# Kernel tuning notes

Hardware: AMD Instinct MI355X
Metric: run time of the kernel (lower is better)

## Reference

```python
import jax, jax.numpy as jnp
import numpy as np

# Module constants (from init_kwargs / MoELayer branch for n_experts=8)
D_MODEL = 512
D_FF = 2048
N_HEADS = 8
N_EXPERTS = 8
TOP_K = 2
CAPACITY_FACTOR = 1.6  # n_experts > 6 branch
BATCH = 4096
SEQ = 16  # 4x4 board
LN_EPS = 1e-5


def setup_inputs() -> dict:
    key = jax.random.key(0)
    ks = jax.random.split(key, 24)
    s = 0.02
    d, f, e = D_MODEL, D_FF, N_EXPERTS
    inp = {
        'x': jax.random.normal(ks[0], (BATCH, SEQ, d), dtype=jnp.float32),
        'ln1_g': jnp.ones((d,), jnp.float32), 'ln1_b': jnp.zeros((d,), jnp.float32),
        'ln2_g': jnp.ones((d,), jnp.float32), 'ln2_b': jnp.zeros((d,), jnp.float32),
        # Linear weights stored [in, out] (equivalent to torch W.T)
        'wq': jax.random.normal(ks[1], (d, d)) * s, 'bq': jnp.zeros((d,)),
        'wk': jax.random.normal(ks[2], (d, d)) * s, 'bk': jnp.zeros((d,)),
        'wv': jax.random.normal(ks[3], (d, d)) * s, 'bv': jnp.zeros((d,)),
        'wo': jax.random.normal(ks[4], (d, d)) * s, 'bo': jnp.zeros((d,)),
        'router_w': jax.random.normal(ks[5], (d, e)) * s, 'router_b': jnp.zeros((e,)),
        'w1': jax.random.normal(ks[6], (e, d, f)) * s, 'b1': jnp.zeros((e, f)),
        'w2': jax.random.normal(ks[7], (e, f, d)) * s, 'b2': jnp.zeros((e, d)),
    }
    return inp


def _layernorm(x, g, b):
    mu = x.mean(-1, keepdims=True)
    var = ((x - mu) ** 2).mean(-1, keepdims=True)
    return (x - mu) * jax.lax.rsqrt(var + LN_EPS) * g + b


def _moe(xf, router_w, router_b, w1, b1, w2, b2):
    # xf: [T, D]
    T = xf.shape[0]
    probs = jax.nn.softmax(xf @ router_w + router_b, axis=-1)  # [T, E]
    _, topk_idx = jax.lax.top_k(probs, TOP_K)                  # [T, K]
    capacity = int(np.ceil(T * CAPACITY_FACTOR / N_EXPERTS))
    out = jnp.zeros_like(xf)
    tok = jnp.arange(T)
    for i in range(N_EXPERTS):
        mask = (topk_idx == i).any(-1)                 # token routed to expert i
        pos = jnp.where(mask, tok, T)                  # sentinel T for unrouted
        sel = jnp.sort(pos)[:capacity]                 # first `capacity` routed tokens, in token order
        xi = xf[jnp.minimum(sel, T - 1)]               # gather (padded rows unused)
        hi = jax.nn.gelu(xi @ w1[i] + b1[i], approximate=False)
        yi = hi @ w2[i] + b2[i]
        # scatter; OOB sentinel indices are dropped. Later experts overwrite
        # earlier ones for tokens routed to multiple experts (matches torch).
        out = out.at[sel].set(yi, mode='drop')
    return out


def reference(x, ln1_g, ln1_b, ln2_g, ln2_b, wq, bq, wk, bk, wv, bv, wo, bo,
              router_w, router_b, w1, b1, w2, b2):
    B, S, D = x.shape
    dk = D // N_HEADS
    # --- attention sublayer ---
    h = _layernorm(x, ln1_g, ln1_b)
    q = (h @ wq + bq).reshape(B, S, N_HEADS, dk)
    k = (h @ wk + bk).reshape(B, S, N_HEADS, dk)
    v = (h @ wv + bv).reshape(B, S, N_HEADS, dk)
    scores = jnp.einsum('bqhd,bkhd->bhqk', q, k) / np.sqrt(dk).astype(np.float32)
    attn = jax.nn.softmax(scores, axis=-1)
    ctx = jnp.einsum('bhqk,bkhd->bqhd', attn, v).reshape(B, S, D)
    x = x + ctx @ wo + bo
    # --- MoE sublayer ---
    h2 = _layernorm(x, ln2_g, ln2_b)
    moe_out = _moe(h2.reshape(-1, D), router_w, router_b, w1, b1, w2, b2)
    return x + moe_out.reshape(B, S, D)
```

## Files before the change

kernel.cpp:

```cpp
#include <hip/hip_runtime.h>
#include <hip/hip_bf16.h>
#include <math.h>

typedef unsigned short u16;
typedef unsigned int u32;
typedef _Float16 f16;
typedef __attribute__((ext_vector_type(8))) _Float16 f16x8;
typedef __attribute__((ext_vector_type(8))) short short8;
typedef __attribute__((ext_vector_type(4))) float f32x4;

#define TTOK 65536
#define QTOK 16384
#define CAP 13108
#define CAPP 13184

#define MFMA16(a, b, c) __builtin_amdgcn_mfma_f32_16x16x32_f16(a, b, c, 0, 0, 0)
#define MFMAB(a, b, c) __builtin_amdgcn_mfma_f32_16x16x32_bf16(a, b, c, 0, 0, 0)
#define LO_SCALE 2.44140625e-4f

#define SWZF(r) (((r) & 3) ^ ((((r) >> 2) & 1) << 1))

__device__ __forceinline__ u16 f2bf(float f) {
  union { float f; u32 u; } v; v.f = f;
  u32 r = v.u + 0x7fffu + ((v.u >> 16) & 1u);
  return (u16)(r >> 16);
}
__device__ __forceinline__ u16 f16b(f16 h) {
  union { f16 h; u16 u; } v; v.h = h; return v.u;
}
__device__ __forceinline__ f16 b2h(u16 u) {
  union { u16 s; f16 h; } v; v.s = u; return v.h;
}
__device__ __forceinline__ float gelu_f(float x) {
  float z = fabsf(x) * 0.70710678118654752f;
  float t = __builtin_amdgcn_rcpf(1.0f + 0.3275911f * z);
  float p = t * (0.254829592f + t * (-0.284496736f + t * (1.421413741f
          + t * (-1.453152027f + t * 1.061405429f))));
  float er = 1.0f - p * __expf(-z * z);
  er = (x < 0.0f) ? -er : er;
  return 0.5f * x * (1.0f + er);
}
__device__ __forceinline__ void gl16(const u16* g, u16* l) {
  __builtin_amdgcn_global_load_lds(
      (const __attribute__((address_space(1))) u32*)(const void*)g,
      (__attribute__((address_space(3))) u32*)(void*)l, 16, 0, 0);
}

__global__ __launch_bounds__(256) void prep1_kernel(
    const float* __restrict__ wq, const float* __restrict__ wk,
    const float* __restrict__ wv, const float* __restrict__ wo,
    const float* __restrict__ rw,
    u16* __restrict__ whi, u16* __restrict__ wlo, float* __restrict__ rwt)
{
  const int z = blockIdx.z;
  int idx = blockIdx.x * 256 + threadIdx.x;
  if (z == 4) {
    if (idx < 4096) {
      int n = idx >> 9, k = idx & 511;
      rwt[idx] = rw[k * 8 + n];
    }
    return;
  }
  const float* src = (z == 0) ? wq : (z == 1) ? wk : (z == 2) ? wv : wo;
  int n = idx >> 9, k = idx & 511;
  float v = src[k * 512 + n];
  f16 h = (f16)v;
  f16 l = (f16)((v - (float)h) * 4096.0f);
  whi[z * 262144 + idx] = f16b(h);
  wlo[z * 262144 + idx] = f16b(l);
}

__global__ __launch_bounds__(256) void prep2_kernel(
    const float* __restrict__ w1, const float* __restrict__ w2,
    u16* __restrict__ w1t, u16* __restrict__ w2t)
{
  __shared__ float tS[64][65];
  const int z = blockIdx.z;
  const float* src; u16* dst; int R, C;
  if (z < 8) { src = w1 + (size_t)z * 1048576; dst = w1t + (size_t)z * 1048576; R = 512; C = 2048; }
  else       { src = w2 + (size_t)(z - 8) * 1048576; dst = w2t + (size_t)(z - 8) * 1048576; R = 2048; C = 512; }
  const int tc = C >> 6;
  const int r0 = (blockIdx.x / tc) * 64, c0 = (blockIdx.x % tc) * 64;
  const int tid = threadIdx.x;
  #pragma unroll
  for (int j = 0; j < 16; ++j) {
    int idx = j * 256 + tid;
    int r = idx >> 6, c = idx & 63;
    tS[r][c] = src[(size_t)(r0 + r) * C + c0 + c];
  }
  __syncthreads();
  #pragma unroll
  for (int j = 0; j < 16; ++j) {
    int idx = j * 256 + tid;
    int c = idx >> 6, r = idx & 63;
    dst[(size_t)(c0 + c) * R + r0 + r] = f2bf(tS[r][c]);
  }
}

__global__ __launch_bounds__(256) void ln1_kernel(
    const float* __restrict__ x, const float* __restrict__ g,
    const float* __restrict__ b, u16* __restrict__ hh, u16* __restrict__ hl)
{
  const int row = blockIdx.x * 4 + (threadIdx.x >> 6);
  const int lane = threadIdx.x & 63;
  const float* xr = x + (size_t)row * 512 + lane * 8;
  float4 a = *(const float4*)xr;
  float4 c = *(const float4*)(xr + 4);
  double s1 = (double)a.x + a.y + a.z + a.w + c.x + c.y + c.z + c.w;
  double s2 = (double)a.x * a.x + (double)a.y * a.y + (double)a.z * a.z + (double)a.w * a.w
            + (double)c.x * c.x + (double)c.y * c.y + (double)c.z * c.z + (double)c.w * c.w;
  #pragma unroll
  for (int off = 32; off; off >>= 1) {
    s1 += __shfl_xor(s1, off, 64);
    s2 += __shfl_xor(s2, off, 64);
  }
  double mu = s1 * (1.0 / 512.0);
  double var = s2 * (1.0 / 512.0) - mu * mu;
  double rs = 1.0 / sqrt(var + 1e-5);
  float4 ga = *(const float4*)(g + lane * 8);
  float4 gb = *(const float4*)(g + lane * 8 + 4);
  float4 ba = *(const float4*)(b + lane * 8);
  float4 bb = *(const float4*)(b + lane * 8 + 4);
  float vv[8] = {a.x, a.y, a.z, a.w, c.x, c.y, c.z, c.w};
  float gg[8] = {ga.x, ga.y, ga.z, ga.w, gb.x, gb.y, gb.z, gb.w};
  float cc[8] = {ba.x, ba.y, ba.z, ba.w, bb.x, bb.y, bb.z, bb.w};
  u16 oh[8], ol[8];
  #pragma unroll
  for (int j = 0; j < 8; ++j) {
    float t = (float)(((double)vv[j] - mu) * rs);
    float n0 = t * gg[j] + cc[j];
    f16 h = (f16)n0;
    oh[j] = f16b(h);
    ol[j] = f16b((f16)((n0 - (float)h) * 4096.0f));
  }
  size_t base = (size_t)row * 512 + lane * 8;
  *(short8*)(hh + base) = *(const short8*)oh;
  *(short8*)(hl + base) = *(const short8*)ol;
}

__device__ __forceinline__ void qkv_body(
    int lid, u16* SMb,
    const u16* __restrict__ hh, const u16* __restrict__ hl,
    const u16* __restrict__ whi, const u16* __restrict__ wlo,
    const float* __restrict__ bq, const float* __restrict__ bk,
    const float* __restrict__ bv, u32* __restrict__ qkvh, int M0)
{
  const int tid = threadIdx.x;
  const int lane = tid & 63, w = tid >> 6;
  const int c8 = lid & 7, kk = lid >> 3;
  const int rt = c8 * 16 + kk / 12;
  const int ct = kk % 12;
  const int col0 = ct * 128;
  const int row0 = rt * 128;
  const int wr = w >> 2, wc = w & 3;
  const int lr = lane & 15, lkq = lane >> 4;
  const int sx = (lkq ^ SWZF(lr)) * 8;
  const int lrow = lane >> 2;
  const int lcs = ((lane & 3) ^ SWZF(lrow)) * 8;

  const u16* gsrc[4];
  int loff[4];
  #pragma unroll
  for (int j = 0; j < 4; ++j) {
    const int q = w * 4 + j;
    loff[j] = q * 512;
    if (q < 8)       gsrc[j] = hh + (size_t)(M0 + row0 + q * 16 + lrow) * 512 + lcs;
    else if (q < 16) gsrc[j] = hl + (size_t)(M0 + row0 + (q - 8) * 16 + lrow) * 512 + lcs;
    else if (q < 24) gsrc[j] = whi + (size_t)(col0 + (q - 16) * 16 + lrow) * 512 + lcs;
    else             gsrc[j] = wlo + (size_t)(col0 + (q - 24) * 16 + lrow) * 512 + lcs;
  }

  f32x4 acch[4][2], accl[4][2];
  #pragma unroll
  for (int m = 0; m < 4; ++m)
    #pragma unroll
    for (int n = 0; n < 2; ++n) {
      f32x4 zz = {0.f, 0.f, 0.f, 0.f};
      acch[m][n] = zz; accl[m][n] = zz;
    }

  #pragma unroll
  for (int j = 0; j < 4; ++j) gl16(gsrc[j], &SMb[loff[j]]);
  #pragma unroll
  for (int j = 0; j < 4; ++j) gl16(gsrc[j] + 32, &SMb[16384 + loff[j]]);

  for (int kc = 0; kc < 16; ++kc) {
    if (kc == 15) asm volatile("s_waitcnt vmcnt(0)" ::: "memory");
    else          asm volatile("s_waitcnt vmcnt(4)" ::: "memory");
    __builtin_amdgcn_s_barrier();
    __builtin_amdgcn_sched_barrier(0);
    const u16* S = &SMb[(kc & 1) * 16384];
    f16x8 ah[4], al[4], bh[2], bl[2];
    #pragma unroll
    for (int m = 0; m < 4; ++m) {
      int r = wr * 64 + m * 16 + lr;
      ah[m] = *(const f16x8*)&S[r * 32 + sx];
      al[m] = *(const f16x8*)&S[4096 + r * 32 + sx];
    }
    #pragma unroll
    for (int n = 0; n < 2; ++n) {
      int c = wc * 32 + n * 16 + lr;
      bh[n] = *(const f16x8*)&S[8192 + c * 32 + sx];
      bl[n] = *(const f16x8*)&S[12288 + c * 32 + sx];
    }
    #pragma unroll
    for (int m = 0; m < 4; ++m)
      #pragma unroll
      for (int n = 0; n < 2; ++n) {
        acch[m][n] = MFMA16(ah[m], bh[n], acch[m][n]);
        accl[m][n] = MFMA16(ah[m], bl[n], accl[m][n]);
        accl[m][n] = MFMA16(al[m], bh[n], accl[m][n]);
      }
    __builtin_amdgcn_s_barrier();
    __builtin_amdgcn_sched_barrier(0);
    if (kc + 2 < 16) {
      #pragma unroll
      for (int j = 0; j < 4; ++j) gl16(gsrc[j] + (kc + 2) * 32, &SMb[(kc & 1) * 16384 + loff[j]]);
    }
  }
  #pragma unroll
  for (int m = 0; m < 4; ++m)
    #pragma unroll
    for (int n = 0; n < 2; ++n) {
      int col = col0 + wc * 32 + n * 16 + lr;
      float bb = (col < 512) ? bq[col] : (col < 1024) ? bk[col - 512] : bv[col - 1024];
      #pragma unroll
      for (int r = 0; r < 4; ++r) {
        int row = row0 + wr * 64 + m * 16 + lkq * 4 + r;
        float val = acch[m][n][r] + accl[m][n][r] * LO_SCALE + bb;
        f16 vh = (f16)val;
        f16 vl = (f16)((val - (float)vh) * 4096.0f);
        qkvh[(size_t)row * 1536 + col] = (u32)f16b(vh) | ((u32)f16b(vl) << 16);
      }
    }
}

__global__ __launch_bounds__(512, 2) void qkv_gemm_kernel(
    const u16* __restrict__ hh, const u16* __restrict__ hl,
    const u16* __restrict__ whi, const u16* __restrict__ wlo,
    const float* __restrict__ bq, const float* __restrict__ bk,
    const float* __restrict__ bv, u32* __restrict__ qkvh, int M0)
{
  __shared__ alignas(16) u16 SM[2][16384];
  qkv_body(blockIdx.x + 12 * blockIdx.y, &SM[0][0],
           hh, hl, whi, wlo, bq, bk, bv, qkvh, M0);
}

__device__ __forceinline__ void wo_body(
    int lid, u16* SMb,
    const u16* __restrict__ cth, const u16* __restrict__ ctl,
    const u16* __restrict__ whi, const u16* __restrict__ wlo,
    const float* __restrict__ bo, const float* __restrict__ x,
    float* __restrict__ dout, int M0)
{
  const int tid = threadIdx.x;
  const int lane = tid & 63, w = tid >> 6;
  const int c8 = lid & 7, kk = lid >> 3;
  const int rt = c8 * 16 + (kk >> 2), ct = kk & 3;
  const int col0 = ct * 128;
  const int row0 = rt * 128;
  const int wr = w >> 2, wc = w & 3;
  const int lr = lane & 15, lkq = lane >> 4;
  const int sx = (lkq ^ SWZF(lr)) * 8;
  const int lrow = lane >> 2;
  const int lcs = ((lane & 3) ^ SWZF(lrow)) * 8;

  const u16* wh3 = whi + 3 * 262144;
  const u16* wl3 = wlo + 3 * 262144;

  const u16* gsrc[4];
  int loff[4];
  #pragma unroll
  for (int j = 0; j < 4; ++j) {
    const int q = w * 4 + j;
    loff[j] = q * 512;
    if (q < 8)       gsrc[j] = cth + (size_t)(row0 + q * 16 + lrow) * 512 + lcs;
    else if (q < 16) gsrc[j] = ctl + (size_t)(row0 + (q - 8) * 16 + lrow) * 512 + lcs;
    else if (q < 24) gsrc[j] = wh3 + (size_t)(col0 + (q - 16) * 16 + lrow) * 512 + lcs;
    else             gsrc[j] = wl3 + (size_t)(col0 + (q - 24) * 16 + lrow) * 512 + lcs;
  }

  f32x4 acch[4][2], accl[4][2];
  #pragma unroll
  for (int m = 0; m < 4; ++m)
    #pragma unroll
    for (int n = 0; n < 2; ++n) {
      f32x4 zz = {0.f, 0.f, 0.f, 0.f};
      acch[m][n] = zz; accl[m][n] = zz;
    }

  #pragma unroll
  for (int j = 0; j < 4; ++j) gl16(gsrc[j], &SMb[loff[j]]);
  #pragma unroll
  for (int j = 0; j < 4; ++j) gl16(gsrc[j] + 32, &SMb[16384 + loff[j]]);

  for (int kc = 0; kc < 16; ++kc) {
    if (kc == 15) asm volatile("s_waitcnt vmcnt(0)" ::: "memory");
    else          asm volatile("s_waitcnt vmcnt(4)" ::: "memory");
    __builtin_amdgcn_s_barrier();
    __builtin_amdgcn_sched_barrier(0);
    const u16* S = &SMb[(kc & 1) * 16384];
    f16x8 ah[4], al[4], bh[2], bl[2];
    #pragma unroll
    for (int m = 0; m < 4; ++m) {
      int r = wr * 64 + m * 16 + lr;
      ah[m] = *(const f16x8*)&S[r * 32 + sx];
      al[m] = *(const f16x8*)&S[4096 + r * 32 + sx];
    }
    #pragma unroll
    for (int n = 0; n < 2; ++n) {
      int c = wc * 32 + n * 16 + lr;
      bh[n] = *(const f16x8*)&S[8192 + c * 32 + sx];
      bl[n] = *(const f16x8*)&S[12288 + c * 32 + sx];
    }
    #pragma unroll
    for (int m = 0; m < 4; ++m)
      #pragma unroll
      for (int n = 0; n < 2; ++n) {
        acch[m][n] = MFMA16(ah[m], bh[n], acch[m][n]);
        accl[m][n] = MFMA16(ah[m], bl[n], accl[m][n]);
        accl[m][n] = MFMA16(al[m], bh[n], accl[m][n]);
      }
    __builtin_amdgcn_s_barrier();
    __builtin_amdgcn_sched_barrier(0);
    if (kc + 2 < 16) {
      #pragma unroll
      for (int j = 0; j < 4; ++j) gl16(gsrc[j] + (kc + 2) * 32, &SMb[(kc & 1) * 16384 + loff[j]]);
    }
  }
  #pragma unroll
  for (int m = 0; m < 4; ++m)
    #pragma unroll
    for (int n = 0; n < 2; ++n) {
      int col = col0 + wc * 32 + n * 16 + lr;
      float bvv = bo[col];
      #pragma unroll
      for (int r = 0; r < 4; ++r) {
        int row = row0 + wr * 64 + m * 16 + lkq * 4 + r;
        float val = acch[m][n][r] + accl[m][n][r] * LO_SCALE + bvv;
        size_t gi = (size_t)(M0 + row) * 512 + col;
        dout[gi] = x[gi] + val;
      }
    }
}

__global__ __launch_bounds__(512, 2) void wo_gemm_kernel(
    const u16* __restrict__ cth, const u16* __restrict__ ctl,
    const u16* __restrict__ whi, const u16* __restrict__ wlo,
    const float* __restrict__ bo, const float* __restrict__ x,
    float* __restrict__ dout, int M0)
{
  __shared__ alignas(16) u16 SM[2][16384];
  wo_body(blockIdx.x + 4 * blockIdx.y, &SM[0][0],
          cth, ctl, whi, wlo, bo, x, dout, M0);
}

__global__ __launch_bounds__(512) void attn_kernel(
    const u32* __restrict__ qkvh, u16* __restrict__ cth, u16* __restrict__ ctl)
{
  __shared__ alignas(16) u32 vS[16384];
  __shared__ float pS[8][16][17];

  const int tid = threadIdx.x;
  const int lane = tid & 63, w = tid >> 6;
  const int lr = lane & 15, lkq = lane >> 4;
  const int row0 = blockIdx.x * 32;

  #pragma unroll
  for (int i = 0; i < 8; ++i) {
    int chunk = w * 8 + i;
    const u32* src = qkvh + (size_t)(row0 + (chunk >> 1)) * 1536 + 1024 + (chunk & 1) * 256 + lane * 4;
    gl16((const u16*)src, (u16*)(vS + chunk * 256));
  }
  __syncthreads();

  const int h4 = w & 3, s = w >> 2;
  #pragma unroll
  for (int g = 0; g < 2; ++g) {
    const int h = g * 4 + h4;
    f16x8 qh[2], ql[2], kh[2], kl[2];
    #pragma unroll
    for (int dc = 0; dc < 2; ++dc) {
      const u32* qp = qkvh + (size_t)(row0 + s * 16 + lr) * 1536 + h * 64 + dc * 32 + lkq * 8;
      const u32* kp = qp + 512;
      uint4 q0 = *(const uint4*)qp, q1 = *(const uint4*)(qp + 4);
      uint4 k0 = *(const uint4*)kp, k1 = *(const uint4*)(kp + 4);
      u32 qu[8] = {q0.x, q0.y, q0.z, q0.w, q1.x, q1.y, q1.z, q1.w};
      u32 ku[8] = {k0.x, k0.y, k0.z, k0.w, k1.x, k1.y, k1.z, k1.w};
      #pragma unroll
      for (int i = 0; i < 8; ++i) {
        qh[dc][i] = b2h((u16)(qu[i] & 0xffffu)); ql[dc][i] = b2h((u16)(qu[i] >> 16));
        kh[dc][i] = b2h((u16)(ku[i] & 0xffffu)); kl[dc][i] = b2h((u16)(ku[i] >> 16));
      }
    }
    f32x4 sh = {0.f, 0.f, 0.f, 0.f}, sl = {0.f, 0.f, 0.f, 0.f};
    #pragma unroll
    for (int dc = 0; dc < 2; ++dc) {
      sh = MFMA16(qh[dc], kh[dc], sh);
      sl = MFMA16(qh[dc], kl[dc], sl);
      sl = MFMA16(ql[dc], kh[dc], sl);
    }
    float p_[4];
    #pragma unroll
    for (int r = 0; r < 4; ++r) {
      float sv = (sh[r] + sl[r] * LO_SCALE) * 0.125f;
      float mx = sv;
      #pragma unroll
      for (int off = 8; off; off >>= 1) mx = fmaxf(mx, __shfl_xor(mx, off, 16));
      float e = expf(sv - mx);
      float su = e;
      #pragma unroll
      for (int off = 8; off; off >>= 1) su += __shfl_xor(su, off, 16);
      p_[r] = e / su;
    }
    #pragma unroll
    for (int r = 0; r < 4; ++r) pS[w][lkq * 4 + r][lr] = p_[r];
    f16x8 pah, pal;
    #pragma unroll
    for (int jj = 0; jj < 8; ++jj) {
      float pv = (lkq < 2) ? pS[w][lr][lkq * 8 + jj] : 0.0f;
      f16 ph = (f16)pv;
      pah[jj] = ph;
      pal[jj] = (f16)((pv - (float)ph) * 4096.0f);
    }
    #pragma unroll
    for (int cf = 0; cf < 4; ++cf) {
      f16x8 vhf, vlf;
      #pragma unroll
      for (int jj = 0; jj < 8; ++jj) {
        u32 u = (lkq < 2) ? vS[(size_t)(s * 16 + lkq * 8 + jj) * 512 + h * 64 + cf * 16 + lr] : 0u;
        vhf[jj] = b2h((u16)(u & 0xffffu));
        vlf[jj] = b2h((u16)(u >> 16));
      }
      f32x4 ch = {0.f, 0.f, 0.f, 0.f}, cl = {0.f, 0.f, 0.f, 0.f};
      ch = MFMA16(pah, vhf, ch);
      cl = MFMA16(pah, vlf, cl);
      cl = MFMA16(pal, vhf, cl);
      #pragma unroll
      for (int r = 0; r < 4; ++r) {
        float cv = ch[r] + cl[r] * LO_SCALE;
        int row = row0 + s * 16 + lkq * 4 + r;
        int d = h * 64 + cf * 16 + lr;
        size_t gi = (size_t)row * 512 + d;
        f16 chv = (f16)cv;
        cth[gi] = f16b(chv);
        ctl[gi] = f16b((f16)((cv - (float)chv) * 4096.0f));
      }
    }
  }
}

__global__ __launch_bounds__(256) void router_kernel(
    const float* __restrict__ xp, const float* __restrict__ g2,
    const float* __restrict__ b2ln, const float* __restrict__ rwt,
    const float* __restrict__ rb, float* __restrict__ stats,
    int* __restrict__ t2, u16* __restrict__ xn)
{
  const int tid = threadIdx.x;
  const int lane = tid & 63, w = tid >> 6;
  const int tok = blockIdx.x * 4 + w;
  const float* xr = xp + (size_t)tok * 512 + lane * 8;
  float4 a = *(const float4*)(xr);
  float4 b = *(const float4*)(xr + 4);
  double s1 = (double)a.x + a.y + a.z + a.w + b.x + b.y + b.z + b.w;
  double s2 = (double)a.x * a.x + (double)a.y * a.y + (double)a.z * a.z + (double)a.w * a.w
            + (double)b.x * b.x + (double)b.y * b.y + (double)b.z * b.z + (double)b.w * b.w;
  #pragma unroll
  for (int off = 32; off; off >>= 1) {
    s1 += __shfl_xor(s1, off, 64);
    s2 += __shfl_xor(s2, off, 64);
  }
  double mu = s1 * (1.0 / 512.0);
  double var = s2 * (1.0 / 512.0) - mu * mu;
  double rs = 1.0 / sqrt(var + 1e-5);
  if (lane == 0) {
    stats[tok * 2] = (float)mu;
    stats[tok * 2 + 1] = (float)rs;
  }
  float4 ga = *(const float4*)(g2 + lane * 8);
  float4 gb = *(const float4*)(g2 + lane * 8 + 4);
  float4 ca = *(const float4*)(b2ln + lane * 8);
  float4 cb = *(const float4*)(b2ln + lane * 8 + 4);
  {
    float muf = (float)mu, rsf = (float)rs;
    u16 ox[8];
    ox[0] = f2bf((a.x - muf) * rsf * ga.x + ca.x);
    ox[1] = f2bf((a.y - muf) * rsf * ga.y + ca.y);
    ox[2] = f2bf((a.z - muf) * rsf * ga.z + ca.z);
    ox[3] = f2bf((a.w - muf) * rsf * ga.w + ca.w);
    ox[4] = f2bf((b.x - muf) * rsf * gb.x + cb.x);
    ox[5] = f2bf((b.y - muf) * rsf * gb.y + cb.y);
    ox[6] = f2bf((b.z - muf) * rsf * gb.z + cb.z);
    ox[7] = f2bf((b.w - muf) * rsf * gb.w + cb.w);
    *(short8*)(xn + (size_t)tok * 512 + lane * 8) = *(const short8*)ox;
  }
  float h[8];
  h[0] = (float)(((double)a.x - mu) * rs * (double)ga.x + (double)ca.x);
  h[1] = (float)(((double)a.y - mu) * rs * (double)ga.y + (double)ca.y);
  h[2] = (float)(((double)a.z - mu) * rs * (double)ga.z + (double)ca.z);
  h[3] = (float)(((double)a.w - mu) * rs * (double)ga.w + (double)ca.w);
  h[4] = (float)(((double)b.x - mu) * rs * (double)gb.x + (double)cb.x);
  h[5] = (float)(((double)b.y - mu) * rs * (double)gb.y + (double)cb.y);
  h[6] = (float)(((double)b.z - mu) * rs * (double)gb.z + (double)cb.z);
  h[7] = (float)(((double)b.w - mu) * rs * (double)gb.w + (double)cb.w);
  double acc[8];
  #pragma unroll
  for (int e = 0; e < 8; ++e) {
    const float* wp = rwt + e * 512 + lane * 8;
    float4 w0 = *(const float4*)wp;
    float4 w1 = *(const float4*)(wp + 4);
    acc[e] = (double)h[0] * (double)w0.x + (double)h[1] * (double)w0.y
           + (double)h[2] * (double)w0.z + (double)h[3] * (double)w0.w
           + (double)h[4] * (double)w1.x + (double)h[5] * (double)w1.y
           + (double)h[6] * (double)w1.z + (double)h[7] * (double)w1.w;
  }
  #pragma unroll
  for (int e = 0; e < 8; ++e) {
    acc[e] += __shfl_xor(acc[e], 8, 64);
    acc[e] += __shfl_xor(acc[e], 16, 64);
    acc[e] += __shfl_xor(acc[e], 32, 64);
  }
  const int b0 = lane & 1, b1 = (lane >> 1) & 1, b2_ = (lane >> 2) & 1;
  double t4[4];
  #pragma unroll
  for (int k = 0; k < 4; ++k) {
    double mine = b0 ? acc[2 * k + 1] : acc[2 * k];
    double send = b0 ? acc[2 * k] : acc[2 * k + 1];
    t4[k] = mine + __shfl_xor(send, 1, 64);
  }
  double u2[2];
  #pragma unroll
  for (int k = 0; k < 2; ++k) {
    double mine = b1 ? t4[2 * k + 1] : t4[2 * k];
    double send = b1 ? t4[2 * k] : t4[2 * k + 1];
    u2[k] = mine + __shfl_xor(send, 2, 64);
  }
  {
    double mine = b2_ ? u2[1] : u2[0];
    double send = b2_ ? u2[0] : u2[1];
    double tot = mine + __shfl_xor(send, 4, 64);
    const int e = lane & 7;
    double lg = tot + (double)rb[e];
    double vv = lg; int ix = e;
    #pragma unroll
    for (int off = 4; off; off >>= 1) {
      double ov = __shfl_xor(vv, off, 8);
      int oi = __shfl_xor(ix, off, 8);
      if (ov > vv || (ov == vv && oi < ix)) { vv = ov; ix = oi; }
    }
    double v2 = (e == ix) ? -1.0e300 : lg; int ix2 = e;
    #pragma unroll
    for (int off = 4; off; off >>= 1) {
      double ov = __shfl_xor(v2, off, 8);
      int oi = __shfl_xor(ix2, off, 8);
      if (ov > v2 || (ov == v2 && oi < ix2)) { v2 = ov; ix2 = oi; }
    }
    if (lane == 0) t2[tok] = ix | (ix2 << 8);
  }
}

__global__ __launch_bounds__(256) void scan1_kernel(
    const int* __restrict__ t2, int* __restrict__ blkcnt, int* __restrict__ ranks)
{
  __shared__ u32 mask[256];
  __shared__ u16 rk[256][8];
  const int t = threadIdx.x, tok = blockIdx.x * 256 + t;
  const int p = t2[tok];
  const int e1 = p & 0xff, e2 = (p >> 8) & 0xff;
  mask[t] = (1u << e1) | (1u << e2);
  __syncthreads();
  if (t < 8) {
    int c = 0;
    for (int i = 0; i < 256; ++i) { rk[i][t] = (u16)c; c += (mask[i] >> t) & 1u; }
    blkcnt[blockIdx.x * 8 + t] = c;
  }
  __syncthreads();
  ranks[tok] = (int)rk[t][e1] | ((int)rk[t][e2] << 16);
}

__global__ void scan2_kernel(const int* __restrict__ blkcnt,
                             int* __restrict__ offs)
{
  const int e = threadIdx.x;
  if (e < 8) {
    int off = 0;
    for (int b = 0; b < 256; ++b) { offs[b * 8 + e] = off; off += blkcnt[b * 8 + e]; }
  }
}

__global__ __launch_bounds__(256) void scan3_kernel(
    const int* __restrict__ t2, const int* __restrict__ ranks,
    const int* __restrict__ offs, int* __restrict__ wblkcnt,
    int* __restrict__ wrk_tok)
{
  __shared__ u32 wmask[256];
  __shared__ u16 wrk[256][8];
  const int t = threadIdx.x, blk = blockIdx.x, tok = blk * 256 + t;
  const int p = t2[tok];
  const int e1 = p & 0xff, e2 = (p >> 8) & 0xff;
  const int r = ranks[tok];
  const int s1 = offs[blk * 8 + e1] + (r & 0xffff);
  const int s2 = offs[blk * 8 + e2] + ((r >> 16) & 0xffff);
  int w = -1;
  if (s1 < CAP) w = (e1 > w) ? e1 : w;
  if (s2 < CAP) w = (e2 > w) ? e2 : w;
  wmask[t] = (w >= 0) ? (1u << w) : 0u;
  __syncthreads();
  if (t < 8) {
    int c = 0;
    for (int i = 0; i < 256; ++i) { wrk[i][t] = (u16)c; c += (wmask[i] >> t) & 1u; }
    wblkcnt[blk * 8 + t] = c;
  }
  __syncthreads();
  wrk_tok[tok] = (w >= 0) ? ((int)wrk[t][w] | (w << 16)) : -1;
}

__global__ void scan4_kernel(const int* __restrict__ wblkcnt,
                             int* __restrict__ woffs, int* __restrict__ wcnt)
{
  const int e = threadIdx.x;
  if (e < 8) {
    int off = 0;
    for (int b = 0; b < 256; ++b) { woffs[b * 8 + e] = off; off += wblkcnt[b * 8 + e]; }
    wcnt[e] = off;
  }
}

__global__ __launch_bounds__(256) void scan5_kernel(
    const int* __restrict__ wrk_tok, const int* __restrict__ woffs,
    int* __restrict__ wlist)
{
  const int t = threadIdx.x, blk = blockIdx.x, tok = blk * 256 + t;
  const int pr = wrk_tok[tok];
  if (pr >= 0) {
    const int w = pr >> 16, rk = pr & 0xffff;
    wlist[w * CAPP + woffs[blk * 8 + w] + rk] = tok;
  }
}

template<int EPI, int NKC, int AST, int BST, int NX>
__device__ __forceinline__ void ffn_body(
    int lid, u16* SMb,
    const u16* __restrict__ A, const u16* __restrict__ Bw,
    const float* __restrict__ bias, u16* __restrict__ outb,
    const int* __restrict__ list, const int* __restrict__ cnts,
    float* __restrict__ dout, int ebase)
{
  const int c8 = lid & 7;
  const int kk = lid >> 3;
  const int wx = kk & (NX - 1);
  const int pr = kk / NX;
  const int wz = pr / 13;
  const int wy = (pr % 13) * 8 + c8;
  if (wy >= 103) return;
  const int ez = wz;
  const int expert = ebase + ez;
  const int cnt = cnts[expert];
  const int row0 = wy * 128;
  if (row0 >= cnt) return;
  const int tid = threadIdx.x;
  const int lane = tid & 63, w = tid >> 6;
  const int colb = wx * 256;
  const int lr = lane & 15, lkq = lane >> 4;
  const int sx = (lkq ^ SWZF(lr)) * 8;
  const int lrow = lane >> 2;
  const int lcs = ((lane & 3) ^ SWZF(lrow)) * 8;

  const u16* Bp = Bw + (size_t)expert * 1048576;

  const u16* gsrc[6];
  int loff[6];
  #pragma unroll
  for (int j = 0; j < 2; ++j) {
    int q = w * 2 + j;
    int arow = row0 + q * 16 + lrow;
    if (EPI == 0) {
      int tok = list[(size_t)expert * CAPP + arow] & 65535;
      gsrc[j] = A + (size_t)tok * 512 + lcs;
    } else {
      gsrc[j] = A + (size_t)ez * CAPP * 2048 + (size_t)arow * AST + lcs;
    }
    loff[j] = q * 512;
  }
  #pragma unroll
  for (int j = 2; j < 6; ++j) {
    int q = w * 4 + (j - 2);
    gsrc[j] = Bp + (size_t)(colb + q * 16 + lrow) * BST + lcs;
    loff[j] = 4096 + q * 512;
  }

  f32x4 acc[8][4];
  #pragma unroll
  for (int m = 0; m < 8; ++m)
    #pragma unroll
    for (int n = 0; n < 4; ++n) {
      f32x4 zz = {0.f, 0.f, 0.f, 0.f};
      acc[m][n] = zz;
    }

  #pragma unroll
  for (int j = 0; j < 6; ++j) gl16(gsrc[j], &SMb[loff[j]]);
  #pragma unroll
  for (int j = 0; j < 6; ++j) gl16(gsrc[j] + 32, &SMb[12288 + loff[j]]);

  int cur = 0, nx2 = 2;
  for (int kc = 0; kc < NKC; ++kc) {
    if (kc == NKC - 1) asm volatile("s_waitcnt vmcnt(0)" ::: "memory");
    else               asm volatile("s_waitcnt vmcnt(6)" ::: "memory");
    __builtin_amdgcn_s_barrier();
    __builtin_amdgcn_sched_barrier(0);
    if (kc + 2 < NKC) {
      #pragma unroll
      for (int j = 0; j < 6; ++j) gl16(gsrc[j] + (kc + 2) * 32, &SMb[nx2 * 12288 + loff[j]]);
    }
    const u16* S = &SMb[cur * 12288];
    short8 af[8], bf[4];
    #pragma unroll
    for (int m = 0; m < 8; ++m)
      af[m] = *(const short8*)&S[(m * 16 + lr) * 32 + sx];
    #pragma unroll
    for (int n = 0; n < 4; ++n)
      bf[n] = *(const short8*)&S[4096 + (w * 64 + n * 16 + lr) * 32 + sx];
    #pragma unroll
    for (int m = 0; m < 8; ++m)
      #pragma unroll
      for (int n = 0; n < 4; ++n)
        acc[m][n] = MFMAB(af[m], bf[n], acc[m][n]);
    cur = (cur == 2) ? 0 : cur + 1;
    nx2 = (nx2 == 2) ? 0 : nx2 + 1;
  }

  if (EPI == 0) {
    #pragma unroll
    for (int m = 0; m < 8; ++m)
      #pragma unroll
      for (int n = 0; n < 4; ++n) {
        int col = colb + w * 64 + n * 16 + lr;
        float bvv = bias[expert * 2048 + col];
        #pragma unroll
        for (int r = 0; r < 4; ++r) {
          int row = row0 + m * 16 + lkq * 4 + r;
          float val = acc[m][n][r] + bvv;
          outb[(size_t)ez * CAPP * 2048 + (size_t)row * 2048 + col] = f2bf(gelu_f(val));
        }
      }
  } else {
    const int* gidx = list + (size_t)expert * CAPP;
    #pragma unroll
    for (int m = 0; m < 8; ++m) {
      int rowb = row0 + m * 16 + lkq * 4;
      #pragma unroll
      for (int r = 0; r < 4; ++r) {
        int row = rowb + r;
        if (row < cnt) {
          int tok = gidx[row];
          #pragma unroll
          for (int n = 0; n < 4; ++n) {
            int col = colb + w * 64 + n * 16 + lr;
            float val = acc[m][n][r] + bias[expert * 512 + col];
            size_t oi = (size_t)tok * 512 + col;
            dout[oi] = dout[oi] + val;
          }
        }
      }
    }
  }
}

__global__ __launch_bounds__(256, 2) void ffn_merged_kernel(
    const u16* __restrict__ xn, const u16* __restrict__ w1t,
    const float* __restrict__ b1, u16* __restrict__ hidW,
    const u16* __restrict__ hidR, const u16* __restrict__ w2t,
    const float* __restrict__ b2,
    const int* __restrict__ wlist, const int* __restrict__ wcnt,
    float* __restrict__ dout, int nb2, int eb1, int eb2)
{
  __shared__ alignas(16) u16 SM[3][12288];
  const int bx = blockIdx.x;
  if (bx < nb2) {
    ffn_body<1, 64, 2048, 2048, 2>(bx, &SM[0][0], hidR, w2t, b2, nullptr,
                                   wlist, wcnt, dout, eb2);
  } else {
    ffn_body<0, 16, 512, 512, 8>(bx - nb2, &SM[0][0], xn, w1t, b1, hidW,
                                 wlist, wcnt, nullptr, eb1);
  }
}

extern "C" void kernel_launch(void* const* d_in, const int* in_sizes, int n_in,
                              void* d_out, int out_size, void* d_ws, size_t ws_size,
                              hipStream_t stream) {
  const float* x    = (const float*)d_in[0];
  const float* ln1g = (const float*)d_in[1];
  const float* ln1b = (const float*)d_in[2];
  const float* ln2g = (const float*)d_in[3];
  const float* ln2b = (const float*)d_in[4];
  const float* wq   = (const float*)d_in[5];
  const float* bq   = (const float*)d_in[6];
  const float* wk   = (const float*)d_in[7];
  const float* bk   = (const float*)d_in[8];
  const float* wv   = (const float*)d_in[9];
  const float* bv   = (const float*)d_in[10];
  const float* wo   = (const float*)d_in[11];
  const float* bo   = (const float*)d_in[12];
  const float* rw   = (const float*)d_in[13];
  const float* rb   = (const float*)d_in[14];
  const float* w1   = (const float*)d_in[15];
  const float* b1   = (const float*)d_in[16];
  const float* w2   = (const float*)d_in[17];
  const float* b2   = (const float*)d_in[18];
  float* dout = (float*)d_out;

  char* ws = (char*)d_ws;
  u16*   hh   = (u16*)(ws + 0LL);
  u16*   hl   = (u16*)(ws + 67108864LL);
  u32*   qkvh = (u32*)(ws + 134217728LL);
  u16*   cth  = (u16*)(ws + 234881024LL);
  u16*   ctl  = (u16*)(ws + 251658240LL);
  u16*   whi  = (u16*)(ws + 369098752LL);
  u16*   wlo  = (u16*)(ws + 371195904LL);
  float* rwt  = (float*)(ws + 373293056LL);
  float* st2  = (float*)(ws + 373309440LL);
  int*   t2   = (int*)(ws + 373833728LL);
  int*   rks  = (int*)(ws + 374095872LL);
  int*   bc   = (int*)(ws + 374358016LL);
  int*   offs = (int*)(ws + 374366208LL);
  int*   wcnt = (int*)(ws + 374374400LL);
  int*   wlst = (int*)(ws + 374374464LL);
  int*   wrkt = (int*)(ws + 374796352LL);
  int*   wbc  = (int*)(ws + 375058496LL);
  int*   wofs = (int*)(ws + 375066688LL);
  u16*   w1t  = (u16*)(ws + 0LL);
  u16*   w2t  = (u16*)(ws + 16777216LL);
  u16*   xn   = (u16*)(ws + 33554432LL);
  u16*   hid0 = (u16*)(ws + 100663296LL);
  u16*   hid1 = (u16*)(ws + 208666624LL);

  prep1_kernel<<<dim3(1024, 1, 5), 256, 0, stream>>>(wq, wk, wv, wo, rw, whi, wlo, rwt);
  ln1_kernel<<<16384, 256, 0, stream>>>(x, ln1g, ln1b, hh, hl);
  for (int q = 0; q < 4; ++q) {
    qkv_gemm_kernel<<<dim3(12, 128), 512, 0, stream>>>(
        hh, hl, whi, wlo, bq, bk, bv, qkvh, q * QTOK);
    attn_kernel<<<512, 512, 0, stream>>>(qkvh, cth, ctl);
    wo_gemm_kernel<<<dim3(4, 128), 512, 0, stream>>>(
        cth, ctl, whi, wlo, bo, x, dout, q * QTOK);
  }
  prep2_kernel<<<dim3(256, 1, 16), 256, 0, stream>>>(w1, w2, w1t, w2t);
  router_kernel<<<16384, 256, 0, stream>>>(dout, ln2g, ln2b, rwt, rb, st2, t2, xn);
  scan1_kernel<<<256, 256, 0, stream>>>(t2, bc, rks);
  scan2_kernel<<<1, 256, 0, stream>>>(bc, offs);
  scan3_kernel<<<256, 256, 0, stream>>>(t2, rks, offs, wbc, wrkt);
  scan4_kernel<<<1, 256, 0, stream>>>(wbc, wofs, wcnt);
  scan5_kernel<<<256, 256, 0, stream>>>(wrkt, wofs, wlst);
  for (int s = 0; s < 5; ++s) {
    const int nb1 = (s < 4) ? 1664 : 0;
    const int nb2 = (s > 0) ? 416 : 0;
    u16* hw = (s & 1) ? hid1 : hid0;
    const u16* hr = ((s - 1) & 1) ? hid1 : hid0;
    ffn_merged_kernel<<<nb1 + nb2, 256, 0, stream>>>(
        xn, w1t, b1, hw, hr, w2t, b2, wlst, wcnt, dout,
        nb2, s * 2, (s - 1) * 2);
  }
}
```

Measured before the change: 1.199 ms.

## Enlarge MoE FFN tiles to 256 rows with 8 waves and double-buffered LDS

```diff
diff --git a/kernel.cpp b/kernel.cpp
--- a/kernel.cpp
+++ b/kernel.cpp
@@ -13,6 +13,7 @@
 #define QTOK 16384
 #define CAP 13108
 #define CAPP 13184
+#define HCAP 13312
 
 #define MFMA16(a, b, c) __builtin_amdgcn_mfma_f32_16x16x32_f16(a, b, c, 0, 0, 0)
 #define MFMAB(a, b, c) __builtin_amdgcn_mfma_f32_16x16x32_bf16(a, b, c, 0, 0, 0)
@@ -650,17 +651,18 @@
   const int kk = lid >> 3;
   const int wx = kk & (NX - 1);
   const int pr = kk / NX;
-  const int wz = pr / 13;
-  const int wy = (pr % 13) * 8 + c8;
-  if (wy >= 103) return;
+  const int wz = pr / 7;
+  const int wy = (pr % 7) * 8 + c8;
+  if (wy >= 52) return;
   const int ez = wz;
   const int expert = ebase + ez;
   const int cnt = cnts[expert];
-  const int row0 = wy * 128;
+  const int row0 = wy * 256;
   if (row0 >= cnt) return;
   const int tid = threadIdx.x;
   const int lane = tid & 63, w = tid >> 6;
   const int colb = wx * 256;
+  const int wr = w >> 2, wc = w & 3;
   const int lr = lane & 15, lkq = lane >> 4;
   const int sx = (lkq ^ SWZF(lr)) * 8;
   const int lrow = lane >> 2;
@@ -668,25 +670,24 @@
 
   const u16* Bp = Bw + (size_t)expert * 1048576;
 
-  const u16* gsrc[6];
-  int loff[6];
-  #pragma unroll
-  for (int j = 0; j < 2; ++j) {
-    int q = w * 2 + j;
-    int arow = row0 + q * 16 + lrow;
-    if (EPI == 0) {
-      int tok = list[(size_t)expert * CAPP + arow] & 65535;
-      gsrc[j] = A + (size_t)tok * 512 + lcs;
+  const u16* gsrc[4];
+  int loff[4];
+  #pragma unroll
+  for (int j = 0; j < 4; ++j) {
+    const int q = w * 4 + j;
+    loff[j] = q * 512;
+    if (q < 16) {
+      int arow = row0 + q * 16 + lrow;
+      if (EPI == 0) {
+        int ai = (arow < CAPP) ? arow : (CAPP - 1);
+        int tok = list[(size_t)expert * CAPP + ai] & 65535;
+        gsrc[j] = A + (size_t)tok * 512 + lcs;
+      } else {
+        gsrc[j] = A + (size_t)ez * HCAP * 2048 + (size_t)arow * AST + lcs;
+      }
     } else {
-      gsrc[j] = A + (size_t)ez * CAPP * 2048 + (size_t)arow * AST + lcs;
-    }
-    loff[j] = q * 512;
-  }
-  #pragma unroll
-  for (int j = 2; j < 6; ++j) {
-    int q = w * 4 + (j - 2);
-    gsrc[j] = Bp + (size_t)(colb + q * 16 + lrow) * BST + lcs;
-    loff[j] = 4096 + q * 512;
+      gsrc[j] = Bp + (size_t)(colb + (q - 16) * 16 + lrow) * BST + lcs;
+    }
   }
 
   f32x4 acc[8][4];
@@ -699,56 +700,55 @@
     }
 
   #pragma unroll
-  for (int j = 0; j < 6; ++j) gl16(gsrc[j], &SMb[loff[j]]);
-  #pragma unroll
-  for (int j = 0; j < 6; ++j) gl16(gsrc[j] + 32, &SMb[12288 + loff[j]]);
-
-  int cur = 0, nx2 = 2;
+  for (int j = 0; j < 4; ++j) gl16(gsrc[j], &SMb[loff[j]]);
+  #pragma unroll
+  for (int j = 0; j < 4; ++j) gl16(gsrc[j] + 32, &SMb[16384 + loff[j]]);
+
   for (int kc = 0; kc < NKC; ++kc) {
     if (kc == NKC - 1) asm volatile("s_waitcnt vmcnt(0)" ::: "memory");
-    else               asm volatile("s_waitcnt vmcnt(6)" ::: "memory");
+    else               asm volatile("s_waitcnt vmcnt(4)" ::: "memory");
+    __builtin_amdgcn_s_barrier();
+    __builtin_amdgcn_sched_barrier(0);
+    const u16* S = &SMb[(kc & 1) * 16384];
+    short8 af[8], bf[4];
+    #pragma unroll
+    for (int m = 0; m < 8; ++m)
+      af[m] = *(const short8*)&S[(wr * 128 + m * 16 + lr) * 32 + sx];
+    #pragma unroll
+    for (int n = 0; n < 4; ++n)
+      bf[n] = *(const short8*)&S[8192 + (wc * 64 + n * 16 + lr) * 32 + sx];
+    #pragma unroll
+    for (int m = 0; m < 8; ++m)
+      #pragma unroll
+      for (int n = 0; n < 4; ++n)
+        acc[m][n] = MFMAB(af[m], bf[n], acc[m][n]);
     __builtin_amdgcn_s_barrier();
     __builtin_amdgcn_sched_barrier(0);
     if (kc + 2 < NKC) {
       #pragma unroll
-      for (int j = 0; j < 6; ++j) gl16(gsrc[j] + (kc + 2) * 32, &SMb[nx2 * 12288 + loff[j]]);
-    }
-    const u16* S = &SMb[cur * 12288];
-    short8 af[8], bf[4];
+      for (int j = 0; j < 4; ++j) gl16(gsrc[j] + (kc + 2) * 32, &SMb[(kc & 1) * 16384 + loff[j]]);
+    }
+  }
+
+  if (EPI == 0) {
     #pragma unroll
     for (int m = 0; m < 8; ++m)
-      af[m] = *(const short8*)&S[(m * 16 + lr) * 32 + sx];
-    #pragma unroll
-    for (int n = 0; n < 4; ++n)
-      bf[n] = *(const short8*)&S[4096 + (w * 64 + n * 16 + lr) * 32 + sx];
-    #pragma unroll
-    for (int m = 0; m < 8; ++m)
-      #pragma unroll
-      for (int n = 0; n < 4; ++n)
-        acc[m][n] = MFMAB(af[m], bf[n], acc[m][n]);
-    cur = (cur == 2) ? 0 : cur + 1;
-    nx2 = (nx2 == 2) ? 0 : nx2 + 1;
-  }
-
-  if (EPI == 0) {
-    #pragma unroll
-    for (int m = 0; m < 8; ++m)
       #pragma unroll
       for (int n = 0; n < 4; ++n) {
-        int col = colb + w * 64 + n * 16 + lr;
+        int col = colb + wc * 64 + n * 16 + lr;
         float bvv = bias[expert * 2048 + col];
         #pragma unroll
         for (int r = 0; r < 4; ++r) {
-          int row = row0 + m * 16 + lkq * 4 + r;
+          int row = row0 + wr * 128 + m * 16 + lkq * 4 + r;
           float val = acc[m][n][r] + bvv;
-          outb[(size_t)ez * CAPP * 2048 + (size_t)row * 2048 + col] = f2bf(gelu_f(val));
+          outb[(size_t)ez * HCAP * 2048 + (size_t)row * 2048 + col] = f2bf(gelu_f(val));
         }
       }
   } else {
     const int* gidx = list + (size_t)expert * CAPP;
     #pragma unroll
     for (int m = 0; m < 8; ++m) {
-      int rowb = row0 + m * 16 + lkq * 4;
+      int rowb = row0 + wr * 128 + m * 16 + lkq * 4;
       #pragma unroll
       for (int r = 0; r < 4; ++r) {
         int row = rowb + r;
@@ -756,7 +756,7 @@
           int tok = gidx[row];
           #pragma unroll
           for (int n = 0; n < 4; ++n) {
-            int col = colb + w * 64 + n * 16 + lr;
+            int col = colb + wc * 64 + n * 16 + lr;
             float val = acc[m][n][r] + bias[expert * 512 + col];
             size_t oi = (size_t)tok * 512 + col;
             dout[oi] = dout[oi] + val;
@@ -767,7 +767,7 @@
   }
 }
 
-__global__ __launch_bounds__(256, 2) void ffn_merged_kernel(
+__global__ __launch_bounds__(512, 2) void ffn_merged_kernel(
     const u16* __restrict__ xn, const u16* __restrict__ w1t,
     const float* __restrict__ b1, u16* __restrict__ hidW,
     const u16* __restrict__ hidR, const u16* __restrict__ w2t,
@@ -775,7 +775,7 @@
     const int* __restrict__ wlist, const int* __restrict__ wcnt,
     float* __restrict__ dout, int nb2, int eb1, int eb2)
 {
-  __shared__ alignas(16) u16 SM[3][12288];
+  __shared__ alignas(16) u16 SM[2][16384];
   const int bx = blockIdx.x;
   if (bx < nb2) {
     ffn_body<1, 64, 2048, 2048, 2>(bx, &SM[0][0], hidR, w2t, b2, nullptr,
@@ -833,7 +833,7 @@
   u16*   w2t  = (u16*)(ws + 16777216LL);
   u16*   xn   = (u16*)(ws + 33554432LL);
   u16*   hid0 = (u16*)(ws + 100663296LL);
-  u16*   hid1 = (u16*)(ws + 208666624LL);
+  u16*   hid1 = (u16*)(ws + 209715200LL);
 
   prep1_kernel<<<dim3(1024, 1, 5), 256, 0, stream>>>(wq, wk, wv, wo, rw, whi, wlo, rwt);
   ln1_kernel<<<16384, 256, 0, stream>>>(x, ln1g, ln1b, hh, hl);
@@ -852,11 +852,11 @@
   scan4_kernel<<<1, 256, 0, stream>>>(wbc, wofs, wcnt);
   scan5_kernel<<<256, 256, 0, stream>>>(wrkt, wofs, wlst);
   for (int s = 0; s < 5; ++s) {
-    const int nb1 = (s < 4) ? 1664 : 0;
-    const int nb2 = (s > 0) ? 416 : 0;
+    const int nb1 = (s < 4) ? 896 : 0;
+    const int nb2 = (s > 0) ? 224 : 0;
     u16* hw = (s & 1) ? hid1 : hid0;
     const u16* hr = ((s - 1) & 1) ? hid1 : hid0;
-    ffn_merged_kernel<<<nb1 + nb2, 256, 0, stream>>>(
+    ffn_merged_kernel<<<nb1 + nb2, 512, 0, stream>>>(
         xn, w1t, b1, hw, hr, w2t, b2, wlst, wcnt, dout,
         nb2, s * 2, (s - 1) * 2);
   }
```

New measurement: 1.212 ms. About the same (+1.1%).

## Compact expert hidden buffer and restructure FFN pipeline into three launches

Applied to the files above, without the earlier changes.

```diff
diff --git a/kernel.cpp b/kernel.cpp
--- a/kernel.cpp
+++ b/kernel.cpp
@@ -624,6 +624,11 @@
     for (int b = 0; b < 256; ++b) { woffs[b * 8 + e] = off; off += wblkcnt[b * 8 + e]; }
     wcnt[e] = off;
   }
+  __syncthreads();
+  if (e == 0) {
+    int p = 0;
+    for (int i = 0; i < 8; ++i) { wcnt[8 + i] = p; p += wcnt[i]; }
+  }
 }
 
 __global__ __launch_bounds__(256) void scan5_kernel(
@@ -653,9 +658,9 @@
   const int wz = pr / 13;
   const int wy = (pr % 13) * 8 + c8;
   if (wy >= 103) return;
-  const int ez = wz;
-  const int expert = ebase + ez;
+  const int expert = ebase + wz;
   const int cnt = cnts[expert];
+  const int hbase = cnts[8 + expert];
   const int row0 = wy * 128;
   if (row0 >= cnt) return;
   const int tid = threadIdx.x;
@@ -678,7 +683,7 @@
       int tok = list[(size_t)expert * CAPP + arow] & 65535;
       gsrc[j] = A + (size_t)tok * 512 + lcs;
     } else {
-      gsrc[j] = A + (size_t)ez * CAPP * 2048 + (size_t)arow * AST + lcs;
+      gsrc[j] = A + (size_t)(hbase + arow) * AST + lcs;
     }
     loff[j] = q * 512;
   }
@@ -740,8 +745,10 @@
         #pragma unroll
         for (int r = 0; r < 4; ++r) {
           int row = row0 + m * 16 + lkq * 4 + r;
-          float val = acc[m][n][r] + bvv;
-          outb[(size_t)ez * CAPP * 2048 + (size_t)row * 2048 + col] = f2bf(gelu_f(val));
+          if (row < cnt) {
+            float val = acc[m][n][r] + bvv;
+            outb[(size_t)(hbase + row) * 2048 + col] = f2bf(gelu_f(val));
+          }
         }
       }
   } else {
@@ -769,19 +776,18 @@
 
 __global__ __launch_bounds__(256, 2) void ffn_merged_kernel(
     const u16* __restrict__ xn, const u16* __restrict__ w1t,
-    const float* __restrict__ b1, u16* __restrict__ hidW,
-    const u16* __restrict__ hidR, const u16* __restrict__ w2t,
-    const float* __restrict__ b2,
+    const float* __restrict__ b1, u16* __restrict__ hid,
+    const u16* __restrict__ w2t, const float* __restrict__ b2,
     const int* __restrict__ wlist, const int* __restrict__ wcnt,
     float* __restrict__ dout, int nb2, int eb1, int eb2)
 {
   __shared__ alignas(16) u16 SM[3][12288];
   const int bx = blockIdx.x;
   if (bx < nb2) {
-    ffn_body<1, 64, 2048, 2048, 2>(bx, &SM[0][0], hidR, w2t, b2, nullptr,
+    ffn_body<1, 64, 2048, 2048, 2>(bx, &SM[0][0], hid, w2t, b2, nullptr,
                                    wlist, wcnt, dout, eb2);
   } else {
-    ffn_body<0, 16, 512, 512, 8>(bx - nb2, &SM[0][0], xn, w1t, b1, hidW,
+    ffn_body<0, 16, 512, 512, 8>(bx - nb2, &SM[0][0], xn, w1t, b1, hid,
                                  wlist, wcnt, nullptr, eb1);
   }
 }
@@ -832,8 +838,7 @@
   u16*   w1t  = (u16*)(ws + 0LL);
   u16*   w2t  = (u16*)(ws + 16777216LL);
   u16*   xn   = (u16*)(ws + 33554432LL);
-  u16*   hid0 = (u16*)(ws + 100663296LL);
-  u16*   hid1 = (u16*)(ws + 208666624LL);
+  u16*   hid  = (u16*)(ws + 100663296LL);
 
   prep1_kernel<<<dim3(1024, 1, 5), 256, 0, stream>>>(wq, wk, wv, wo, rw, whi, wlo, rwt);
   ln1_kernel<<<16384, 256, 0, stream>>>(x, ln1g, ln1b, hh, hl);
@@ -851,13 +856,10 @@
   scan3_kernel<<<256, 256, 0, stream>>>(t2, rks, offs, wbc, wrkt);
   scan4_kernel<<<1, 256, 0, stream>>>(wbc, wofs, wcnt);
   scan5_kernel<<<256, 256, 0, stream>>>(wrkt, wofs, wlst);
-  for (int s = 0; s < 5; ++s) {
-    const int nb1 = (s < 4) ? 1664 : 0;
-    const int nb2 = (s > 0) ? 416 : 0;
-    u16* hw = (s & 1) ? hid1 : hid0;
-    const u16* hr = ((s - 1) & 1) ? hid1 : hid0;
-    ffn_merged_kernel<<<nb1 + nb2, 256, 0, stream>>>(
-        xn, w1t, b1, hw, hr, w2t, b2, wlst, wcnt, dout,
-        nb2, s * 2, (s - 1) * 2);
-  }
-}
+  ffn_merged_kernel<<<3328, 256, 0, stream>>>(
+      xn, w1t, b1, hid, w2t, b2, wlst, wcnt, dout, 0, 0, 0);
+  ffn_merged_kernel<<<832 + 3328, 256, 0, stream>>>(
+      xn, w1t, b1, hid, w2t, b2, wlst, wcnt, dout, 832, 4, 0);
+  ffn_merged_kernel<<<832, 256, 0, stream>>>(
+      xn, w1t, b1, hid, w2t, b2, wlst, wcnt, dout, 832, 0, 4);
+}
```

Result: slower. 1.284 ms (+7.1%).
